# Performance work log

Hardware: AMD Instinct MI355X
Metric: run time of the kernel (lower is better)

Reference implementation:

```python
import jax, jax.numpy as jnp
import numpy as np

N_QUBITS = 12
N_LAYERS = 3
N_PARAMS = N_QUBITS * 3 * N_LAYERS  # 108
BATCH = 8192
DIM = 1 << N_QUBITS  # 4096


def _rx(theta):
    c = jnp.cos(theta / 2).astype(jnp.complex64)
    s = jnp.sin(theta / 2).astype(jnp.complex64)
    return jnp.stack([jnp.stack([c, -1j * s]), jnp.stack([-1j * s, c])])


def _ry(theta):
    c = jnp.cos(theta / 2).astype(jnp.complex64)
    s = jnp.sin(theta / 2).astype(jnp.complex64)
    return jnp.stack([jnp.stack([c, -s]), jnp.stack([s, c])])


def _rz(theta):
    e = jnp.exp(-1j * theta.astype(jnp.complex64) / 2)
    z = jnp.zeros((), jnp.complex64)
    return jnp.stack([jnp.stack([e, z]), jnp.stack([z, jnp.conj(e)])])


def _apply_1q(state, q, U):
    # state: (B,) + (2,)*n ; apply 2x2 gate U on wire q (axis q+1)
    s = jnp.moveaxis(state, q + 1, -1)
    s = s @ U.T
    return jnp.moveaxis(s, -1, q + 1)


def _cnot(state, c, t):
    # control wire c, target wire t (axes offset by 1 for batch dim)
    ca, ta = c + 1, t + 1
    s0 = jax.lax.index_in_dim(state, 0, ca, keepdims=False)
    s1 = jax.lax.index_in_dim(state, 1, ca, keepdims=False)
    ta2 = ta - 1 if ta > ca else ta  # target axis shifts after removing control axis
    s1 = jnp.flip(s1, axis=ta2)  # X on target (size-2 axis)
    return jnp.stack([s0, s1], axis=ca)


def setup_inputs() -> dict:
    key = jax.random.key(0)
    k1, k2 = jax.random.split(key)
    x = jax.random.normal(k1, (BATCH, DIM), dtype=jnp.float32)
    params = jax.random.normal(k2, (N_PARAMS,), dtype=jnp.float32) * 0.1
    return {"x": x, "params": params}


def reference(x, params):
    n = N_QUBITS
    B = x.shape[0]
    # AmplitudeEmbedding with normalize=True
    norm = jnp.linalg.norm(x, axis=1, keepdims=True)
    state = (x / norm).astype(jnp.complex64).reshape((B,) + (2,) * n)
    idx = 0
    for _ in range(N_LAYERS):
        for q in range(n):
            state = _apply_1q(state, q, _rx(params[idx])); idx += 1
            state = _apply_1q(state, q, _ry(params[idx])); idx += 1
            state = _apply_1q(state, q, _rz(params[idx])); idx += 1
        for q in range(n):
            state = _cnot(state, q, (q + 1) % n)
    # <Z_q> = P(q=0) - P(q=1)
    p = state.real ** 2 + state.imag ** 2  # (B,) + (2,)*n, float32
    outs = []
    for q in range(n):
        axes = tuple(a for a in range(1, n + 1) if a != q + 1)
        marg = jnp.sum(p, axis=axes)  # (B, 2)
        outs.append(marg[:, 0] - marg[:, 1])
    return jnp.stack(outs, axis=1)  # (B, n_qubits)
```

## Files before the change

### kernel.cpp

```cpp
#include <hip/hip_runtime.h>
#include <math.h>

#define NQ 12
#define DIM 4096
#define NGATES 36
#define NROUND 9

typedef float f32x4 __attribute__((ext_vector_type(4)));
typedef __fp16 fp16x2 __attribute__((ext_vector_type(2)));
typedef __fp16 fp16x4 __attribute__((ext_vector_type(4)));
typedef __fp16 fp16x8 __attribute__((ext_vector_type(8)));

constexpr unsigned swz(unsigned x) { return x ^ (x >> 4); }

struct Round {
  unsigned s[4];
  unsigned l[4];
  unsigned cbsw8[16];
  unsigned dt[4];
};
struct PlanT {
  Round rd[NROUND];
  unsigned zsel[NQ];
};

constexpr PlanT make_plan() {
  PlanT P{};
  unsigned Mcol[NQ] = {}, Minv[NQ] = {};
  for (int i = 0; i < NQ; ++i) { Mcol[i] = 1u << i; Minv[i] = 1u << i; }
  unsigned gm[NGATES] = {}, gs[NGATES] = {};
  int g = 0;
  for (int L = 0; L < 3; ++L) {
    for (int q = 0; q < NQ; ++q) { int b = NQ - 1 - q; gm[g] = Mcol[b]; gs[g] = Minv[b]; ++g; }
    for (int q = 0; q < NQ; ++q) {
      int bc = NQ - 1 - q, bt = NQ - 1 - ((q + 1) % NQ);
      Mcol[bc] ^= Mcol[bt];
      Minv[bt] ^= Minv[bc];
    }
  }
  for (int r = 0; r < NROUND; ++r) {
    unsigned m[4], red[4];
    for (int k = 0; k < 4; ++k) { m[k] = gm[4*r+k]; red[k] = m[k]; P.rd[r].s[k] = gs[4*r+k]; }
    for (int a = 0; a < 4; ++a) {
      unsigned p = red[a] & (0u - red[a]);
      for (int b = a + 1; b < 4; ++b) if (red[b] & p) red[b] ^= red[a];
    }
    unsigned piv[4];
    for (int a = 0; a < 4; ++a) piv[a] = red[a] & (0u - red[a]);
    for (int a = 0; a < 4; ++a)
      for (int b = a + 1; b < 4; ++b)
        if (piv[a] > piv[b]) { unsigned tp = piv[a]; piv[a] = piv[b]; piv[b] = tp; }
    for (int a = 0; a < 4; ++a) P.rd[r].l[a] = piv[a] - 1u;
    for (int d = 0; d < 16; ++d) {
      unsigned c = 0;
      for (int k = 0; k < 4; ++k) if (d & (1 << k)) c ^= m[k];
      P.rd[r].cbsw8[d] = swz(c) << 3;
    }
    for (int tt = 0; tt < 4; ++tt) {
      unsigned c = (unsigned)tt << 4;
      unsigned j = c;
      j = ((j & ~P.rd[r].l[0]) << 1) | (j & P.rd[r].l[0]);
      j = ((j & ~P.rd[r].l[1]) << 1) | (j & P.rd[r].l[1]);
      j = ((j & ~P.rd[r].l[2]) << 1) | (j & P.rd[r].l[2]);
      j = ((j & ~P.rd[r].l[3]) << 1) | (j & P.rd[r].l[3]);
      unsigned d = swz(j) << 3;
      for (int k = 0; k < 4; ++k)
        if (__builtin_popcount(j & P.rd[r].s[k]) & 1) d ^= P.rd[r].cbsw8[1u << k];
      P.rd[r].dt[tt] = d;
    }
  }
  for (int q = 0; q < NQ; ++q) P.zsel[q] = Minv[NQ - 1 - q];
  return P;
}

constexpr PlanT PLAN = make_plan();

__global__ void qc_prep(const float* __restrict__ params, __fp16* __restrict__ amat) {
  int t = threadIdx.x;
  int r = t >> 4, s = t & 15;
  if (r >= NROUND) return;
  float U[4][8];
  for (int k = 0; k < 4; ++k) {
    int gg = r * 4 + k;
    float h1 = params[3*gg+0]*0.5f, hh2 = params[3*gg+1]*0.5f, h3 = params[3*gg+2]*0.5f;
    float c1 = cosf(h1), s1 = sinf(h1);
    float c2 = cosf(hh2), s2 = sinf(hh2);
    float c3 = cosf(h3), s3 = sinf(h3);
    float a00r =  c2*c1, a00i =  s2*s1;
    float a01r = -s2*c1, a01i = -c2*s1;
    float a10r =  s2*c1, a10i = -c2*s1;
    float a11r =  c2*c1, a11i = -s2*s1;
    U[k][0] = c3*a00r + s3*a00i;  U[k][1] = c3*a00i - s3*a00r;
    U[k][2] = c3*a01r + s3*a01i;  U[k][3] = c3*a01i - s3*a01r;
    U[k][4] = c3*a10r - s3*a10i;  U[k][5] = c3*a10i + s3*a10r;
    U[k][6] = c3*a11r - s3*a11i;  U[k][7] = c3*a11i + s3*a11r;
  }
  __fp16* b0 = amat + r*2048 + s*32;
  __fp16* b1 = b0 + 512;
  __fp16* b2 = b0 + 1024;
  __fp16* b3 = b0 + 1536;
  for (int j = 0; j < 16; ++j) {
    float pr = 1.f, pi = 0.f;
    for (int k = 0; k < 4; ++k) {
      int idx = ((((s >> k) & 1) * 2) + ((j >> k) & 1)) * 2;
      float gr = U[k][idx], gi = U[k][idx + 1];
      float npr = pr * gr - pi * gi;
      pi = pr * gi + pi * gr;
      pr = npr;
    }
    float v0_ =  pr; __fp16 e0 = (__fp16)v0_;
    float v1_ = -pi; __fp16 e1 = (__fp16)v1_;
    float v2_ =  pi; __fp16 e2 = (__fp16)v2_;
    float v3_ =  pr; __fp16 e3 = (__fp16)v3_;
    b0[2*j]   = e0;  b1[2*j]   = (__fp16)(v0_ - (float)e0);
    b0[2*j+1] = e1;  b1[2*j+1] = (__fp16)(v1_ - (float)e1);
    b2[2*j]   = e2;  b3[2*j]   = (__fp16)(v2_ - (float)e2);
    b2[2*j+1] = e3;  b3[2*j+1] = (__fp16)(v3_ - (float)e3);
  }
}

__global__ __launch_bounds__(256)
__attribute__((amdgpu_waves_per_eu(4, 5)))
void qc_main(const float* __restrict__ x, const __fp16* __restrict__ amat,
             float* __restrict__ out) {
  __shared__ float2 sst[DIM];
  char* sb = (char*)sst;
  float* sf = (float*)sst;
  const int t = threadIdx.x;
  const long row = blockIdx.x;

  const float4* x4 = (const float4*)(x + (size_t)row * DIM);
  float ssq = 0.f;
#pragma unroll
  for (int k = 0; k < 4; ++k) {
    float4 a = x4[t + 256*k];
    int j0 = 4*(t + 256*k);
    *(float2*)(sb + (swz((unsigned)j0)     << 3)) = make_float2(a.x, 0.f);
    *(float2*)(sb + (swz((unsigned)(j0+1)) << 3)) = make_float2(a.y, 0.f);
    *(float2*)(sb + (swz((unsigned)(j0+2)) << 3)) = make_float2(a.z, 0.f);
    *(float2*)(sb + (swz((unsigned)(j0+3)) << 3)) = make_float2(a.w, 0.f);
    ssq += a.x*a.x + a.y*a.y + a.z*a.z + a.w*a.w;
  }
#pragma unroll
  for (int off = 32; off > 0; off >>= 1) ssq += __shfl_down(ssq, off, 64);
  __syncthreads();

#pragma unroll 1
  for (int r = 0; r < NROUND; ++r) {
    const unsigned s0 = PLAN.rd[r].s[0], sA = PLAN.rd[r].s[1];
    const unsigned sB = PLAN.rd[r].s[2], sC = PLAN.rd[r].s[3];
    const unsigned l0 = PLAN.rd[r].l[0], l1 = PLAN.rd[r].l[1];
    const unsigned l2 = PLAN.rd[r].l[2], l3 = PLAN.rd[r].l[3];
    const unsigned CB1 = PLAN.rd[r].cbsw8[1], CB2 = PLAN.rd[r].cbsw8[2];
    const unsigned CB3 = PLAN.rd[r].cbsw8[3];
    const unsigned C4 = PLAN.rd[r].cbsw8[4], C8 = PLAN.rd[r].cbsw8[8];
    const unsigned D1 = PLAN.rd[r].dt[1], D2 = PLAN.rd[r].dt[2];
    const unsigned D3 = PLAN.rd[r].dt[3];

    unsigned j = ((unsigned)t & 0xC0u) | ((unsigned)t & 15u);
    j = ((j & ~l0) << 1) | (j & l0);
    j = ((j & ~l1) << 1) | (j & l1);
    j = ((j & ~l2) << 1) | (j & l2);
    j = ((j & ~l3) << 1) | (j & l3);
    unsigned adj8 = 0;
    adj8 ^= (unsigned)(-(int)(__popc(j & s0) & 1)) & CB1;
    adj8 ^= (unsigned)(-(int)(__popc(j & sA) & 1)) & CB2;
    adj8 ^= (unsigned)(-(int)(__popc(j & sB) & 1)) & C4;
    adj8 ^= (unsigned)(-(int)(__popc(j & sC) & 1)) & C8;
    const unsigned q = ((unsigned)t >> 4) & 3u;
    const unsigned qsel = ((q & 1u) ? C4 : 0u) ^ ((q & 2u) ? C8 : 0u);
    const unsigned b0a = (((j ^ (j >> 4)) << 3) ^ adj8) ^ qsel;

    const fp16x8* am = (const fp16x8*)(amat + (size_t)r * 2048);
    const int fo = (t & 15) * 4 + (int)q;
    const fp16x8 Arh = am[fo];
    const fp16x8 Arl = am[64 + fo];
    const fp16x8 Aih = am[128 + fo];
    const fp16x8 Ail = am[192 + fo];

#pragma unroll
    for (int tt = 0; tt < 4; ++tt) {
      const unsigned bb = b0a ^ (tt == 0 ? 0u : tt == 1 ? D1 : tt == 2 ? D2 : D3);
      const unsigned a0 = bb, a1 = bb ^ CB1, a2 = bb ^ CB2, a3 = bb ^ CB3;
      const float2 A0 = *(const float2*)(sb + a0);
      const float2 A1 = *(const float2*)(sb + a1);
      const float2 A2 = *(const float2*)(sb + a2);
      const float2 A3 = *(const float2*)(sb + a3);
      fp16x2 p0 = __builtin_amdgcn_cvt_pkrtz(A0.x, A0.y);
      fp16x2 p1 = __builtin_amdgcn_cvt_pkrtz(A1.x, A1.y);
      fp16x2 p2 = __builtin_amdgcn_cvt_pkrtz(A2.x, A2.y);
      fp16x2 p3 = __builtin_amdgcn_cvt_pkrtz(A3.x, A3.y);
      fp16x2 q0 = __builtin_amdgcn_cvt_pkrtz(A0.x - (float)p0[0], A0.y - (float)p0[1]);
      fp16x2 q1 = __builtin_amdgcn_cvt_pkrtz(A1.x - (float)p1[0], A1.y - (float)p1[1]);
      fp16x2 q2 = __builtin_amdgcn_cvt_pkrtz(A2.x - (float)p2[0], A2.y - (float)p2[1]);
      fp16x2 q3 = __builtin_amdgcn_cvt_pkrtz(A3.x - (float)p3[0], A3.y - (float)p3[1]);
      fp16x4 u01 = __builtin_shufflevector(p0, p1, 0, 1, 2, 3);
      fp16x4 u23 = __builtin_shufflevector(p2, p3, 0, 1, 2, 3);
      fp16x8 Bhi = __builtin_shufflevector(u01, u23, 0, 1, 2, 3, 4, 5, 6, 7);
      fp16x4 w01 = __builtin_shufflevector(q0, q1, 0, 1, 2, 3);
      fp16x4 w23 = __builtin_shufflevector(q2, q3, 0, 1, 2, 3);
      fp16x8 Blo = __builtin_shufflevector(w01, w23, 0, 1, 2, 3, 4, 5, 6, 7);

      f32x4 are = {0.f, 0.f, 0.f, 0.f}, aim = {0.f, 0.f, 0.f, 0.f};
      are = __builtin_amdgcn_mfma_f32_16x16x32_f16(Arh, Bhi, are, 0, 0, 0);
      are = __builtin_amdgcn_mfma_f32_16x16x32_f16(Arl, Bhi, are, 0, 0, 0);
      are = __builtin_amdgcn_mfma_f32_16x16x32_f16(Arh, Blo, are, 0, 0, 0);
      are = __builtin_amdgcn_mfma_f32_16x16x32_f16(Arl, Blo, are, 0, 0, 0);
      aim = __builtin_amdgcn_mfma_f32_16x16x32_f16(Aih, Bhi, aim, 0, 0, 0);
      aim = __builtin_amdgcn_mfma_f32_16x16x32_f16(Ail, Bhi, aim, 0, 0, 0);
      aim = __builtin_amdgcn_mfma_f32_16x16x32_f16(Aih, Blo, aim, 0, 0, 0);
      aim = __builtin_amdgcn_mfma_f32_16x16x32_f16(Ail, Blo, aim, 0, 0, 0);

      *(float2*)(sb + a0) = make_float2(are[0], aim[0]);
      *(float2*)(sb + a1) = make_float2(are[1], aim[1]);
      *(float2*)(sb + a2) = make_float2(are[2], aim[2]);
      *(float2*)(sb + a3) = make_float2(are[3], aim[3]);
    }
    __syncthreads();
  }

  const unsigned mbase8 = (((16u * (unsigned)t) ^ (unsigned)t) << 3);
  float p[16];
#pragma unroll
  for (int c = 0; c < 16; ++c) {
    float2 v = *(const float2*)(sb + (mbase8 ^ ((unsigned)c << 3)));
    p[c] = v.x * v.x + v.y * v.y;
  }
#pragma unroll
  for (int b = 0; b < 4; ++b) {
#pragma unroll
    for (int c = 0; c < 16; ++c) {
      if (!(c & (1 << b))) {
        const int c1 = c | (1 << b);
        float u = p[c], v = p[c1];
        p[c] = u + v; p[c1] = u - v;
      }
    }
  }
  float zs[NQ];
#pragma unroll
  for (int qq = 0; qq < NQ; ++qq) {
    const unsigned m = PLAN.zsel[qq];
    const float v = p[m & 15u];
    const int sgn = __popc((unsigned)t & (m >> 4)) & 1;
    zs[qq] = sgn ? -v : v;
  }
#pragma unroll
  for (int qq = 0; qq < NQ; ++qq) {
#pragma unroll
    for (int off = 32; off > 0; off >>= 1) zs[qq] += __shfl_down(zs[qq], off, 64);
  }
  __syncthreads();
  const int w = t >> 6;
  if ((t & 63) == 0) {
#pragma unroll
    for (int qq = 0; qq < NQ; ++qq) sf[w*NQ + qq] = zs[qq];
    sf[48 + w] = ssq;
  }
  __syncthreads();
  if (t < NQ) {
    const float den = sf[48] + sf[49] + sf[50] + sf[51];
    const float tot = sf[t] + sf[NQ + t] + sf[2*NQ + t] + sf[3*NQ + t];
    out[row * NQ + t] = tot / den;
  }
}

extern "C" void kernel_launch(void* const* d_in, const int* in_sizes, int n_in,
                              void* d_out, int out_size, void* d_ws, size_t ws_size,
                              hipStream_t stream) {
  const float* x = (const float*)d_in[0];
  const float* params = (const float*)d_in[1];
  float* out = (float*)d_out;
  __fp16* amat = (__fp16*)d_ws;
  const int nrows = in_sizes[0] / DIM;
  qc_prep<<<dim3(1), dim3(256), 0, stream>>>(params, amat);
  qc_main<<<dim3(nrows), dim3(256), 0, stream>>>(x, amat, out);
}
```

Measured before the change: 327.2 us.

## Drop low*low MFMA terms and replace shuffle reductions with LDS tree reduction

Removes the lo×lo fp16 split-precision MFMA products for both the real and imaginary parts, cutting the matrix-core work per gate round by a quarter at a small precision cost. It also replaces the 12 per-qubit 64-lane shuffle reductions with a staged LDS reduction: each thread writes its partial sums to shared memory, then 192 threads sum strided slices and finish with 32-lane shuffles. This is meant to cut cross-lane shuffle traffic in the epilogue, in exchange for an extra shared-memory pass.

```diff
diff --git a/kernel.cpp b/kernel.cpp
--- a/kernel.cpp
+++ b/kernel.cpp
@@ -125,7 +125,6 @@
              float* __restrict__ out) {
   __shared__ float2 sst[DIM];
   char* sb = (char*)sst;
-  float* sf = (float*)sst;
   const int t = threadIdx.x;
   const long row = blockIdx.x;
 
@@ -205,11 +204,9 @@
       are = __builtin_amdgcn_mfma_f32_16x16x32_f16(Arh, Bhi, are, 0, 0, 0);
       are = __builtin_amdgcn_mfma_f32_16x16x32_f16(Arl, Bhi, are, 0, 0, 0);
       are = __builtin_amdgcn_mfma_f32_16x16x32_f16(Arh, Blo, are, 0, 0, 0);
-      are = __builtin_amdgcn_mfma_f32_16x16x32_f16(Arl, Blo, are, 0, 0, 0);
       aim = __builtin_amdgcn_mfma_f32_16x16x32_f16(Aih, Bhi, aim, 0, 0, 0);
       aim = __builtin_amdgcn_mfma_f32_16x16x32_f16(Ail, Bhi, aim, 0, 0, 0);
       aim = __builtin_amdgcn_mfma_f32_16x16x32_f16(Aih, Blo, aim, 0, 0, 0);
-      aim = __builtin_amdgcn_mfma_f32_16x16x32_f16(Ail, Blo, aim, 0, 0, 0);
 
       *(float2*)(sb + a0) = make_float2(are[0], aim[0]);
       *(float2*)(sb + a1) = make_float2(are[1], aim[1]);
@@ -245,23 +242,35 @@
     const int sgn = __popc((unsigned)t & (m >> 4)) & 1;
     zs[qq] = sgn ? -v : v;
   }
-#pragma unroll
-  for (int qq = 0; qq < NQ; ++qq) {
-#pragma unroll
-    for (int off = 32; off > 0; off >>= 1) zs[qq] += __shfl_down(zs[qq], off, 64);
-  }
-  __syncthreads();
-  const int w = t >> 6;
-  if ((t & 63) == 0) {
-#pragma unroll
-    for (int qq = 0; qq < NQ; ++qq) sf[w*NQ + qq] = zs[qq];
-    sf[48 + w] = ssq;
+
+  __syncthreads();
+#pragma unroll
+  for (int k = 0; k < 6; ++k)
+    *(float2*)(sb + (((unsigned)(k << 8) + (unsigned)t) << 3)) =
+        make_float2(zs[2*k], zs[2*k+1]);
+  if ((t & 63) == 0) *(float*)(sb + 12288 + (t >> 6) * 4) = ssq;
+  __syncthreads();
+  if (t < 192) {
+    const int k = t >> 5, j = t & 31;
+    const char* cbp = sb + (k << 11) + (j << 3);
+    float2 acc = *(const float2*)(cbp);
+#pragma unroll
+    for (int i = 1; i < 8; ++i) {
+      float2 vv = *(const float2*)(cbp + i * 256);
+      acc.x += vv.x; acc.y += vv.y;
+    }
+#pragma unroll
+    for (int off = 16; off > 0; off >>= 1) {
+      acc.x += __shfl_down(acc.x, off, 32);
+      acc.y += __shfl_down(acc.y, off, 32);
+    }
+    if (j == 0) *(float2*)(sb + 12352 + (k << 3)) = acc;
   }
   __syncthreads();
   if (t < NQ) {
-    const float den = sf[48] + sf[49] + sf[50] + sf[51];
-    const float tot = sf[t] + sf[NQ + t] + sf[2*NQ + t] + sf[3*NQ + t];
-    out[row * NQ + t] = tot / den;
+    const float* sq = (const float*)(sb + 12288);
+    const float den = sq[0] + sq[1] + sq[2] + sq[3];
+    out[row * NQ + t] = ((const float*)(sb + 12352))[t] / den;
   }
 }
 
```

After: 302.3 us. 1.08x faster.
